# Kernel tuning notes

Hardware: AMD Instinct MI355X
Metric: run time of the kernel (lower is better)

## Reference

```python
import jax, jax.numpy as jnp
import numpy as np

HIDDEN = 2048
HEADS = 16
HEAD_DIM = HIDDEN // HEADS  # 128
SCALE = 1.0 / float(np.sqrt(HEAD_DIM))
B, S = 2, 2048


def setup_inputs() -> dict:
    key = jax.random.key(0)
    ks = jax.random.split(key, 5)
    return {
        "x": jax.random.normal(ks[0], (B, S, HIDDEN), dtype=jnp.float32),
        "q_w": jax.random.normal(ks[1], (HIDDEN, HIDDEN), dtype=jnp.float32) * (HIDDEN ** -0.5),
        "k_w": jax.random.normal(ks[2], (HEAD_DIM, HIDDEN), dtype=jnp.float32) * (HIDDEN ** -0.5),
        "v_w": jax.random.normal(ks[3], (HEAD_DIM, HIDDEN), dtype=jnp.float32) * (HIDDEN ** -0.5),
        "o_w": jax.random.normal(ks[4], (HIDDEN, HIDDEN), dtype=jnp.float32) * (HIDDEN ** -0.5),
    }


def reference(x, q_w, k_w, v_w, o_w):
    b, s, _ = x.shape
    # torch F.linear: x @ W^T with W [out, in]
    q = (x @ q_w.T).reshape(b, s, HEADS, HEAD_DIM).transpose(0, 2, 1, 3)  # [B,H,S,D]
    k = x @ k_w.T  # [B,S,D] single shared KV head
    v = x @ v_w.T  # [B,S,D]
    # scores: [B,H,S,S] -- explicit O(S^2) materialization as in the source
    scores = jnp.einsum('bhqd,bkd->bhqk', q, k) * SCALE
    # softmax in float32 then cast back (matches dtype=torch.float32 then type_as)
    attn = jax.nn.softmax(scores.astype(jnp.float32), axis=-1).astype(q.dtype)
    out = jnp.einsum('bhqk,bkd->bhqd', attn, v)  # [B,H,S,D]
    out = out.transpose(0, 2, 1, 3).reshape(b, s, HIDDEN)
    return out @ o_w.T
```

## Files before the change

kernel.cpp:

```cpp
#include <hip/hip_runtime.h>
#include <stdint.h>

#define HID 2048
#define DHEAD 128
#define SEQL 2048
#define C2 0.1275187981510609f
#define MOFF 8.0f

typedef __attribute__((ext_vector_type(4))) float f32x4;
typedef __attribute__((ext_vector_type(8))) short s16x8;
typedef __attribute__((ext_vector_type(2))) unsigned int u32x2;

__device__ __forceinline__ unsigned short bf16_rne(float f) {
  union { float f; unsigned u; } v; v.f = f;
  return (unsigned short)((v.u + 0x7FFFu + ((v.u >> 16) & 1u)) >> 16);
}

__device__ __forceinline__ void gload_lds16(const void* g, void* l) {
  __builtin_amdgcn_global_load_lds(
      (__attribute__((address_space(1))) unsigned int*)(void*)g,
      (__attribute__((address_space(3))) unsigned int*)l, 16, 0, 0);
}

__device__ __forceinline__ void cvt8(const float* __restrict__ in,
                                     unsigned short* __restrict__ out, int k) {
  const f32x4* p = (const f32x4*)in;
  f32x4 a = p[2 * k], b = p[2 * k + 1];
  union { s16x8 v; unsigned short s[8]; } o;
  o.s[0] = bf16_rne(a[0]); o.s[1] = bf16_rne(a[1]);
  o.s[2] = bf16_rne(a[2]); o.s[3] = bf16_rne(a[3]);
  o.s[4] = bf16_rne(b[0]); o.s[5] = bf16_rne(b[1]);
  o.s[6] = bf16_rne(b[2]); o.s[7] = bf16_rne(b[3]);
  ((s16x8*)out)[k] = o.v;
}

__global__ __launch_bounds__(256) void cvt_bf16_k(const float* __restrict__ in,
                                                  unsigned short* __restrict__ out,
                                                  int n8) {
  int i = blockIdx.x * 256 + threadIdx.x;
  if (i >= n8) return;
  cvt8(in, out, i);
}

__global__ __launch_bounds__(256) void cvt4_k(
    const float* __restrict__ s0, unsigned short* __restrict__ d0, int n0,
    const float* __restrict__ s1, unsigned short* __restrict__ d1, int n1,
    const float* __restrict__ s2, unsigned short* __restrict__ d2, int n2,
    const float* __restrict__ s3, unsigned short* __restrict__ d3, int n3) {
  int i = blockIdx.x * 256 + threadIdx.x;
  if (i < n0) { cvt8(s0, d0, i); return; }
  i -= n0;
  if (i < n1) { cvt8(s1, d1, i); return; }
  i -= n1;
  if (i < n2) { cvt8(s2, d2, i); return; }
  i -= n2;
  if (i < n3) { cvt8(s3, d3, i); return; }
}

template <int LOG2SLOTS>
__device__ __forceinline__ void stage_tile(const unsigned short* __restrict__ src,
                                           int ld, char* smem, int t) {
  int w = t >> 6;
#pragma unroll
  for (int i = 0; i < 4; ++i) {
    int c = i * 256 + t;
    int row = c >> LOG2SLOTS;
    int slot = c & ((1 << LOG2SLOTS) - 1);
    gload_lds16(src + row * ld + ((slot ^ (row & 7)) << 3),
                smem + (i * 256 + w * 64) * 16);
  }
}

template <int MODE>
__global__ __launch_bounds__(256, 2) void gemm_bt(
    const unsigned short* __restrict__ A, const unsigned short* __restrict__ Bw,
    void* __restrict__ Cout, int M, int N, int K,
    unsigned short* __restrict__ Kb, unsigned short* __restrict__ Vt) {
  __shared__ char As[2][16384];
  __shared__ char Bs[2][16384];
  int t = threadIdx.x;
  int lane = t & 63, w = t >> 6;
  int wm = w >> 1, wn = w & 1;
  int l15 = lane & 15, l4 = lane >> 4;

  int gdx = gridDim.x;
  int nwg = gdx * gridDim.y;
  int bid = blockIdx.y * gdx + blockIdx.x;
  int q8 = nwg >> 3;
  int swz = (bid & 7) * q8 + (bid >> 3);
  int tm = (swz / gdx) * 128, tn = (swz % gdx) * 128;

  f32x4 acc[4][4] = {};

  stage_tile<3>(A + tm * K, K, As[0], t);
  stage_tile<3>(Bw + tn * K, K, Bs[0], t);
  stage_tile<3>(A + tm * K + 64, K, As[1], t);
  stage_tile<3>(Bw + tn * K + 64, K, Bs[1], t);

  int nk = K >> 6;
  for (int ki = 0; ki < nk; ++ki) {
    int cur = ki & 1;
    if (ki < nk - 1) asm volatile("s_waitcnt vmcnt(8)" ::: "memory");
    else             asm volatile("s_waitcnt vmcnt(0)" ::: "memory");
    __builtin_amdgcn_sched_barrier(0);
    __builtin_amdgcn_s_barrier();

    const char* as = As[cur];
    const char* bs = Bs[cur];
    s16x8 af[4][2], bfr[4][2];
#pragma unroll
    for (int m = 0; m < 4; ++m)
#pragma unroll
      for (int kk = 0; kk < 2; ++kk) {
        int row = wm * 64 + m * 16 + l15;
        af[m][kk] = *(const s16x8*)(as + row * 128 + (((kk * 4 + l4) ^ (row & 7)) << 4));
      }
#pragma unroll
    for (int n = 0; n < 4; ++n)
#pragma unroll
      for (int kk = 0; kk < 2; ++kk) {
        int row = wn * 64 + n * 16 + l15;
        bfr[n][kk] = *(const s16x8*)(bs + row * 128 + (((kk * 4 + l4) ^ (row & 7)) << 4));
      }
    asm volatile("s_waitcnt lgkmcnt(0)" ::: "memory");
    __builtin_amdgcn_sched_barrier(0);
    __builtin_amdgcn_s_barrier();
    if (ki + 2 < nk) {
      stage_tile<3>(A + tm * K + (ki + 2) * 64, K, As[cur], t);
      stage_tile<3>(Bw + tn * K + (ki + 2) * 64, K, Bs[cur], t);
    }
    __builtin_amdgcn_s_setprio(1);
#pragma unroll
    for (int m = 0; m < 4; ++m)
#pragma unroll
      for (int n = 0; n < 4; ++n)
#pragma unroll
        for (int kk = 0; kk < 2; ++kk)
          acc[m][n] = __builtin_amdgcn_mfma_f32_16x16x32_bf16(af[m][kk], bfr[n][kk],
                                                              acc[m][n], 0, 0, 0);
    __builtin_amdgcn_s_setprio(0);
  }

#pragma unroll
  for (int m = 0; m < 4; ++m)
#pragma unroll
    for (int n = 0; n < 4; ++n) {
      int col = tn + wn * 64 + n * 16 + l15;
#pragma unroll
      for (int j = 0; j < 4; ++j) {
        int row = tm + wm * 64 + m * 16 + l4 * 4 + j;
        float v = acc[m][n][j];
        if (MODE == 1) {
          ((float*)Cout)[row * N + col] = v;
        } else {
          if (col < 2048) {
            ((unsigned short*)Cout)[row * 2048 + col] = bf16_rne(v);
          } else if (col < 2176) {
            Kb[row * 128 + (col - 2048)] = bf16_rne(v);
          } else {
            int d = col - 2176, bb = row >> 11, s = row & 2047;
            Vt[((bb * 128 + d) << 11) + s] = bf16_rne(v);
          }
        }
      }
    }
}

__global__ __launch_bounds__(256, 2) void attn_k(
    const unsigned short* __restrict__ Q, const unsigned short* __restrict__ Kb,
    const unsigned short* __restrict__ Vt, unsigned short* __restrict__ AO) {
  __shared__ char Ks[2][16384];
  __shared__ char Vs[2][16384];
  __shared__ char Ps[4][4096];
  int t = threadIdx.x;
  int lane = t & 63, w = t >> 6;
  int l15 = lane & 15, l4 = lane >> 4;
  int qt = blockIdx.x, bh = blockIdx.y;
  int b = bh >> 4, h = bh & 15;
  int qg = b * SEQL + qt * 128 + w * 32;
  char* Psw = Ps[w];

  s16x8 qf[2][4];
#pragma unroll
  for (int m = 0; m < 2; ++m)
#pragma unroll
    for (int kc = 0; kc < 4; ++kc)
      qf[m][kc] = *(const s16x8*)(Q + (qg + m * 16 + l15) * HID + h * DHEAD + kc * 32 + l4 * 8);

  union { s16x8 v; unsigned short s[8]; } one_;
#pragma unroll
  for (int i = 0; i < 8; ++i) one_.s[i] = 0x3F80;
  const s16x8 ones = one_.v;

  f32x4 oacc[2][9] = {};

#pragma unroll
  for (int i = 0; i < 4; ++i) {
    int c = i * 256 + t, row = c >> 4, slot = c & 15;
    gload_lds16(Kb + (b * SEQL + row) * DHEAD + ((slot ^ (row & 7)) << 3),
                Ks[0] + (i * 256 + w * 64) * 16);
  }
#pragma unroll
  for (int i = 0; i < 4; ++i) {
    int c = i * 256 + t, row = c >> 3, slot = c & 7;
    gload_lds16(Vt + (b * DHEAD + row) * SEQL + ((slot ^ (row & 7)) << 3),
                Vs[0] + (i * 256 + w * 64) * 16);
  }
  asm volatile("s_waitcnt vmcnt(0)" ::: "memory");
  __builtin_amdgcn_s_barrier();

  for (int kv = 0; kv < SEQL; kv += 64) {
    int cur = (kv >> 6) & 1;
    if (kv + 64 < SEQL) {
#pragma unroll
      for (int i = 0; i < 4; ++i) {
        int c = i * 256 + t, row = c >> 4, slot = c & 15;
        gload_lds16(Kb + (b * SEQL + kv + 64 + row) * DHEAD + ((slot ^ (row & 7)) << 3),
                    Ks[cur ^ 1] + (i * 256 + w * 64) * 16);
      }
#pragma unroll
      for (int i = 0; i < 4; ++i) {
        int c = i * 256 + t, row = c >> 3, slot = c & 7;
        gload_lds16(Vt + (b * DHEAD + row) * SEQL + kv + 64 + ((slot ^ (row & 7)) << 3),
                    Vs[cur ^ 1] + (i * 256 + w * 64) * 16);
      }
    }

    const char* ks = Ks[cur];
    const char* vs = Vs[cur];

    f32x4 sacc[4][2] = {};
    __builtin_amdgcn_s_setprio(1);
#pragma unroll
    for (int n = 0; n < 4; ++n) {
      int krow = n * 16 + l15;
#pragma unroll
      for (int kc = 0; kc < 4; ++kc) {
        s16x8 kf = *(const s16x8*)(ks + krow * 256 + (((kc * 4 + l4) ^ (krow & 7)) << 4));
        sacc[n][0] = __builtin_amdgcn_mfma_f32_16x16x32_bf16(kf, qf[0][kc], sacc[n][0], 0, 0, 0);
        sacc[n][1] = __builtin_amdgcn_mfma_f32_16x16x32_bf16(kf, qf[1][kc], sacc[n][1], 0, 0, 0);
      }
    }
    __builtin_amdgcn_s_setprio(0);

#pragma unroll
    for (int m = 0; m < 2; ++m) {
      int q = m * 16 + l15;
      char* rowp = Psw + q * 128;
      int qx = q & 7;
#pragma unroll
      for (int n = 0; n < 4; ++n) {
        float p0 = __builtin_amdgcn_exp2f(__builtin_fmaf(sacc[n][m][0], C2, -MOFF));
        float p1 = __builtin_amdgcn_exp2f(__builtin_fmaf(sacc[n][m][1], C2, -MOFF));
        float p2 = __builtin_amdgcn_exp2f(__builtin_fmaf(sacc[n][m][2], C2, -MOFF));
        float p3 = __builtin_amdgcn_exp2f(__builtin_fmaf(sacc[n][m][3], C2, -MOFF));
        u32x2 pk;
        pk[0] = (unsigned)bf16_rne(p0) | ((unsigned)bf16_rne(p1) << 16);
        pk[1] = (unsigned)bf16_rne(p2) | ((unsigned)bf16_rne(p3) << 16);
        int off = (((2 * n + (l4 >> 1)) ^ qx) << 4) + ((l4 & 1) << 3);
        *(u32x2*)(rowp + off) = pk;
      }
    }

    asm volatile("s_waitcnt lgkmcnt(0)" ::: "memory");
    __builtin_amdgcn_sched_barrier(0);

#pragma unroll
    for (int kc2 = 0; kc2 < 2; ++kc2) {
      s16x8 pa[2];
#pragma unroll
      for (int m = 0; m < 2; ++m) {
        int row = m * 16 + l15;
        pa[m] = *(const s16x8*)(Psw + row * 128 + (((kc2 * 4 + l4) ^ (row & 7)) << 4));
      }
      __builtin_amdgcn_s_setprio(1);
#pragma unroll
      for (int n = 0; n < 8; ++n) {
        int vrow = n * 16 + l15;
        s16x8 vf = *(const s16x8*)(vs + vrow * 128 + (((kc2 * 4 + l4) ^ (vrow & 7)) << 4));
        oacc[0][n] = __builtin_amdgcn_mfma_f32_16x16x32_bf16(pa[0], vf, oacc[0][n], 0, 0, 0);
        oacc[1][n] = __builtin_amdgcn_mfma_f32_16x16x32_bf16(pa[1], vf, oacc[1][n], 0, 0, 0);
      }
      oacc[0][8] = __builtin_amdgcn_mfma_f32_16x16x32_bf16(pa[0], ones, oacc[0][8], 0, 0, 0);
      oacc[1][8] = __builtin_amdgcn_mfma_f32_16x16x32_bf16(pa[1], ones, oacc[1][8], 0, 0, 0);
      __builtin_amdgcn_s_setprio(0);
    }

    asm volatile("s_waitcnt vmcnt(0) lgkmcnt(0)" ::: "memory");
    __builtin_amdgcn_sched_barrier(0);
    __builtin_amdgcn_s_barrier();
  }

#pragma unroll
  for (int m = 0; m < 2; ++m) {
    float inv[4];
#pragma unroll
    for (int j = 0; j < 4; ++j) inv[j] = 1.f / oacc[m][8][j];
#pragma unroll
    for (int n = 0; n < 8; ++n) {
      int col = h * DHEAD + n * 16 + l15;
#pragma unroll
      for (int j = 0; j < 4; ++j) {
        int row = qg + m * 16 + l4 * 4 + j;
        AO[row * HID + col] = bf16_rne(oacc[m][n][j] * inv[j]);
      }
    }
  }
}

extern "C" void kernel_launch(void* const* d_in, const int* in_sizes, int n_in,
                              void* d_out, int out_size, void* d_ws, size_t ws_size,
                              hipStream_t stream) {
  const float* x  = (const float*)d_in[0];
  const float* qw = (const float*)d_in[1];
  const float* kw = (const float*)d_in[2];
  const float* vw = (const float*)d_in[3];
  const float* ow = (const float*)d_in[4];

  char* ws = (char*)d_ws;
  unsigned short* xb   = (unsigned short*)(ws);
  unsigned short* qwb  = (unsigned short*)(ws + 16777216);
  unsigned short* owb  = qwb;
  unsigned short* kvwb = (unsigned short*)(ws + 25165824);
  unsigned short* Qb   = (unsigned short*)(ws + 26214400);
  unsigned short* Kbuf = (unsigned short*)(ws + 42991616);
  unsigned short* Vtb  = (unsigned short*)(ws + 44040192);
  unsigned short* AOb  = xb;

  cvt4_k<<<6400, 256, 0, stream>>>(x, xb, 1048576, qw, qwb, 524288,
                                   kw, kvwb, 32768, vw, kvwb + 262144, 32768);

  gemm_bt<0><<<dim3(18, 32), 256, 0, stream>>>(xb, qwb, Qb, 4096, 2304, 2048, Kbuf, Vtb);
  cvt_bf16_k<<<2048, 256, 0, stream>>>(ow, owb, 524288);
  attn_k<<<dim3(16, 32), 256, 0, stream>>>(Qb, Kbuf, Vtb, AOb);
  gemm_bt<1><<<dim3(16, 32), 256, 0, stream>>>(AOb, owb, d_out, 4096, 2048, 2048,
                                               nullptr, nullptr);
}
```

Measured before the change: 198.0 us.

## Use 8 waves per GEMM block and fuse o_w conversion when workspace allows

The GEMM kernel moves from 4 waves (2x2, each 64x64) to 8 waves (2x4, each 64x32) per 128x128 tile. Staging is redistributed over 512 threads and the vmcnt wait is adjusted to match. This halves per-wave accumulators and aims to raise occupancy and latency hiding, at the cost of more LDS fragment reads per MFMA. Separately, when the workspace is large enough, the o_w fp32-to-bf16 conversion is folded into the first conversion launch using a dedicated buffer, removing one kernel launch.

```diff
diff --git a/kernel.cpp b/kernel.cpp
--- a/kernel.cpp
+++ b/kernel.cpp
@@ -57,22 +57,38 @@
   if (i < n3) { cvt8(s3, d3, i); return; }
 }
 
-template <int LOG2SLOTS>
-__device__ __forceinline__ void stage_tile(const unsigned short* __restrict__ src,
-                                           int ld, char* smem, int t) {
-  int w = t >> 6;
-#pragma unroll
-  for (int i = 0; i < 4; ++i) {
-    int c = i * 256 + t;
-    int row = c >> LOG2SLOTS;
-    int slot = c & ((1 << LOG2SLOTS) - 1);
+__global__ __launch_bounds__(256) void cvt5_k(
+    const float* __restrict__ s0, unsigned short* __restrict__ d0, int n0,
+    const float* __restrict__ s1, unsigned short* __restrict__ d1, int n1,
+    const float* __restrict__ s2, unsigned short* __restrict__ d2, int n2,
+    const float* __restrict__ s3, unsigned short* __restrict__ d3, int n3,
+    const float* __restrict__ s4, unsigned short* __restrict__ d4, int n4) {
+  int i = blockIdx.x * 256 + threadIdx.x;
+  if (i < n0) { cvt8(s0, d0, i); return; }
+  i -= n0;
+  if (i < n1) { cvt8(s1, d1, i); return; }
+  i -= n1;
+  if (i < n2) { cvt8(s2, d2, i); return; }
+  i -= n2;
+  if (i < n3) { cvt8(s3, d3, i); return; }
+  i -= n3;
+  if (i < n4) { cvt8(s4, d4, i); return; }
+}
+
+__device__ __forceinline__ void stage_tile512(const unsigned short* __restrict__ src,
+                                              int ld, char* smem, int t) {
+#pragma unroll
+  for (int i = 0; i < 2; ++i) {
+    int c = i * 512 + t;
+    int row = c >> 3;
+    int slot = c & 7;
     gload_lds16(src + row * ld + ((slot ^ (row & 7)) << 3),
-                smem + (i * 256 + w * 64) * 16);
+                smem + (i * 512 + (t >> 6) * 64) * 16);
   }
 }
 
 template <int MODE>
-__global__ __launch_bounds__(256, 2) void gemm_bt(
+__global__ __launch_bounds__(512, 4) void gemm_bt(
     const unsigned short* __restrict__ A, const unsigned short* __restrict__ Bw,
     void* __restrict__ Cout, int M, int N, int K,
     unsigned short* __restrict__ Kb, unsigned short* __restrict__ Vt) {
@@ -80,7 +96,7 @@
   __shared__ char Bs[2][16384];
   int t = threadIdx.x;
   int lane = t & 63, w = t >> 6;
-  int wm = w >> 1, wn = w & 1;
+  int wm = w >> 2, wn = w & 3;
   int l15 = lane & 15, l4 = lane >> 4;
 
   int gdx = gridDim.x;
@@ -90,24 +106,24 @@
   int swz = (bid & 7) * q8 + (bid >> 3);
   int tm = (swz / gdx) * 128, tn = (swz % gdx) * 128;
 
-  f32x4 acc[4][4] = {};
-
-  stage_tile<3>(A + tm * K, K, As[0], t);
-  stage_tile<3>(Bw + tn * K, K, Bs[0], t);
-  stage_tile<3>(A + tm * K + 64, K, As[1], t);
-  stage_tile<3>(Bw + tn * K + 64, K, Bs[1], t);
+  f32x4 acc[4][2] = {};
+
+  stage_tile512(A + tm * K, K, As[0], t);
+  stage_tile512(Bw + tn * K, K, Bs[0], t);
+  stage_tile512(A + tm * K + 64, K, As[1], t);
+  stage_tile512(Bw + tn * K + 64, K, Bs[1], t);
 
   int nk = K >> 6;
   for (int ki = 0; ki < nk; ++ki) {
     int cur = ki & 1;
-    if (ki < nk - 1) asm volatile("s_waitcnt vmcnt(8)" ::: "memory");
+    if (ki < nk - 1) asm volatile("s_waitcnt vmcnt(4)" ::: "memory");
     else             asm volatile("s_waitcnt vmcnt(0)" ::: "memory");
     __builtin_amdgcn_sched_barrier(0);
     __builtin_amdgcn_s_barrier();
 
     const char* as = As[cur];
     const char* bs = Bs[cur];
-    s16x8 af[4][2], bfr[4][2];
+    s16x8 af[4][2], bfr[2][2];
 #pragma unroll
     for (int m = 0; m < 4; ++m)
 #pragma unroll
@@ -116,24 +132,24 @@
         af[m][kk] = *(const s16x8*)(as + row * 128 + (((kk * 4 + l4) ^ (row & 7)) << 4));
       }
 #pragma unroll
-    for (int n = 0; n < 4; ++n)
+    for (int n = 0; n < 2; ++n)
 #pragma unroll
       for (int kk = 0; kk < 2; ++kk) {
-        int row = wn * 64 + n * 16 + l15;
+        int row = wn * 32 + n * 16 + l15;
         bfr[n][kk] = *(const s16x8*)(bs + row * 128 + (((kk * 4 + l4) ^ (row & 7)) << 4));
       }
     asm volatile("s_waitcnt lgkmcnt(0)" ::: "memory");
     __builtin_amdgcn_sched_barrier(0);
     __builtin_amdgcn_s_barrier();
     if (ki + 2 < nk) {
-      stage_tile<3>(A + tm * K + (ki + 2) * 64, K, As[cur], t);
-      stage_tile<3>(Bw + tn * K + (ki + 2) * 64, K, Bs[cur], t);
+      stage_tile512(A + tm * K + (ki + 2) * 64, K, As[cur], t);
+      stage_tile512(Bw + tn * K + (ki + 2) * 64, K, Bs[cur], t);
     }
     __builtin_amdgcn_s_setprio(1);
 #pragma unroll
     for (int m = 0; m < 4; ++m)
 #pragma unroll
-      for (int n = 0; n < 4; ++n)
+      for (int n = 0; n < 2; ++n)
 #pragma unroll
         for (int kk = 0; kk < 2; ++kk)
           acc[m][n] = __builtin_amdgcn_mfma_f32_16x16x32_bf16(af[m][kk], bfr[n][kk],
@@ -144,8 +160,8 @@
 #pragma unroll
   for (int m = 0; m < 4; ++m)
 #pragma unroll
-    for (int n = 0; n < 4; ++n) {
-      int col = tn + wn * 64 + n * 16 + l15;
+    for (int n = 0; n < 2; ++n) {
+      int col = tn + wn * 32 + n * 16 + l15;
 #pragma unroll
       for (int j = 0; j < 4; ++j) {
         int row = tm + wm * 64 + m * 16 + l4 * 4 + j;
@@ -320,19 +336,29 @@
   char* ws = (char*)d_ws;
   unsigned short* xb   = (unsigned short*)(ws);
   unsigned short* qwb  = (unsigned short*)(ws + 16777216);
-  unsigned short* owb  = qwb;
   unsigned short* kvwb = (unsigned short*)(ws + 25165824);
   unsigned short* Qb   = (unsigned short*)(ws + 26214400);
   unsigned short* Kbuf = (unsigned short*)(ws + 42991616);
   unsigned short* Vtb  = (unsigned short*)(ws + 44040192);
   unsigned short* AOb  = xb;
 
-  cvt4_k<<<6400, 256, 0, stream>>>(x, xb, 1048576, qw, qwb, 524288,
-                                   kw, kvwb, 32768, vw, kvwb + 262144, 32768);
-
-  gemm_bt<0><<<dim3(18, 32), 256, 0, stream>>>(xb, qwb, Qb, 4096, 2304, 2048, Kbuf, Vtb);
-  cvt_bf16_k<<<2048, 256, 0, stream>>>(ow, owb, 524288);
+  bool big = ws_size >= 54525953ull;
+  unsigned short* owb = big ? (unsigned short*)(ws + 46137344) : qwb;
+
+  if (big) {
+    cvt5_k<<<8448, 256, 0, stream>>>(x, xb, 1048576, qw, qwb, 524288,
+                                     kw, kvwb, 32768, vw, kvwb + 262144, 32768,
+                                     ow, owb, 524288);
+  } else {
+    cvt4_k<<<6400, 256, 0, stream>>>(x, xb, 1048576, qw, qwb, 524288,
+                                     kw, kvwb, 32768, vw, kvwb + 262144, 32768);
+  }
+
+  gemm_bt<0><<<dim3(18, 32), 512, 0, stream>>>(xb, qwb, Qb, 4096, 2304, 2048, Kbuf, Vtb);
+  if (!big) {
+    cvt_bf16_k<<<2048, 256, 0, stream>>>(ow, owb, 524288);
+  }
   attn_k<<<dim3(16, 32), 256, 0, stream>>>(Qb, Kbuf, Vtb, AOb);
-  gemm_bt<1><<<dim3(16, 32), 256, 0, stream>>>(AOb, owb, d_out, 4096, 2048, 2048,
+  gemm_bt<1><<<dim3(16, 32), 512, 0, stream>>>(AOb, owb, d_out, 4096, 2048, 2048,
                                                nullptr, nullptr);
 }
```

After: 195.0 us. No clear change (-1.5%).
